# Kernel optimization log

Measured on AMD Instinct MI355X. Metric: run time of the kernel, lower is better.

The kernel has to match this reference:

```python
import jax, jax.numpy as jnp
import numpy as np

B, S, D, H = 4, 2048, 1024, 16
DH = D // H  # head dim = 64


def setup_inputs() -> dict:
    key = jax.random.key(0)
    ks = jax.random.split(key, 7)
    q = jax.random.normal(ks[0], (B, S, D), dtype=jnp.float32)
    k = jax.random.normal(ks[1], (B, S, D), dtype=jnp.float32)
    v = jax.random.normal(ks[2], (B, S, D), dtype=jnp.float32)
    mask = jax.random.uniform(ks[3], (1, S, S), dtype=jnp.float32)
    sc = 1.0 / np.sqrt(D)
    Wq = jax.random.normal(ks[4], (D, D), dtype=jnp.float32) * sc
    Wk = jax.random.normal(ks[5], (D, D), dtype=jnp.float32) * sc
    Wv = jax.random.normal(ks[6], (D, D), dtype=jnp.float32) * sc
    return {"q": q, "k": k, "v": v, "mask": mask, "Wq": Wq, "Wk": Wk, "Wv": Wv}


def reference(q, k, v, mask, Wq, Wk, Wv):
    # Linear projections (no bias), then split hidden into H heads.
    # tf.concat(tf.split(x, H, axis=2), axis=0) == reshape to (B,S,H,DH);
    # the final split/concat restores channel order [head0, head1, ...],
    # i.e. a plain (B,S,H,DH)->(B,S,D) reshape.
    qh = (q @ Wq).reshape(B, S, H, DH)
    kh = (k @ Wk).reshape(B, S, H, DH)
    vh = (v @ Wv).reshape(B, S, H, DH)
    score = jnp.einsum("bqhd,bkhd->bhqk", qh, kh) / jnp.sqrt(
        jnp.asarray(DH, dtype=q.dtype))
    # multiplicative mask applied BEFORE softmax (broadcast (1,Sq,Sk))
    score = score * mask[:, None, :, :][0:1].squeeze(0) if False else score * mask  # mask (1,Sq,Sk) broadcasts over (B,H,Sq,Sk)
    attn = jax.nn.softmax(score, axis=-1)
    out = jnp.einsum("bhqk,bkhd->bqhd", attn, vh).reshape(B, S, D)
    return out
```

## Files before the change

### kernel.cpp

```cpp
#include <hip/hip_runtime.h>

#define B_  4
#define S_  2048
#define D_  1024
#define H_  16
#define DH_ 64

typedef __attribute__((ext_vector_type(8))) short bf16x8;
typedef __attribute__((ext_vector_type(4))) float f32x4;
typedef __attribute__((ext_vector_type(4))) unsigned short u16x4;

__device__ __forceinline__ unsigned short f2bf(float f) {
  union { float f; unsigned int u; } x; x.f = f;
  unsigned int u = x.u;
  unsigned int r = (u + 0x7fffu + ((u >> 16) & 1u)) >> 16;
  return (unsigned short)r;
}

__device__ __forceinline__ int cvtpk(float lo, float hi) {
  unsigned r;
  asm("v_cvt_pk_bf16_f32 %0, %1, %2" : "=v"(r) : "v"(lo), "v"(hi));
  return (int)r;
}
__device__ __forceinline__ float bperm_f(int addr, float v) {
  union { float f; int i; } x; x.f = v;
  x.i = __builtin_amdgcn_ds_bpermute(addr, x.i);
  return x.f;
}

__global__ __launch_bounds__(256) void wtrans_kernel(const float* __restrict__ W0,
                                                     const float* __restrict__ W1,
                                                     const float* __restrict__ W2,
                                                     unsigned short* __restrict__ Wt) {
  __shared__ float t[32][33];
  const int z = blockIdx.z;
  const float* W = (z == 0) ? W0 : ((z == 1) ? W1 : W2);
  unsigned short* O = Wt + (size_t)z * (D_ * D_);
  const int n0 = blockIdx.x * 32, k0 = blockIdx.y * 32;
  const int tx = threadIdx.x, ty = threadIdx.y;
#pragma unroll
  for (int i = 0; i < 4; i++) t[ty + i * 8][tx] = W[(size_t)(k0 + ty + i * 8) * D_ + n0 + tx];
  __syncthreads();
#pragma unroll
  for (int i = 0; i < 4; i++)
    O[(size_t)(n0 + ty + i * 8) * D_ + k0 + tx] = f2bf(t[tx][ty + i * 8]);
}

__global__ __launch_bounds__(256) void proj_kernel(const float* __restrict__ X0,
                                                   const float* __restrict__ X1,
                                                   const float* __restrict__ X2,
                                                   const unsigned short* __restrict__ Wt,
                                                   unsigned short* __restrict__ Y0) {
  __shared__ unsigned short Alds[128 * 72];
  __shared__ unsigned short Blds[128 * 72];
  const int z = blockIdx.z;
  const float* X = (z == 0) ? X0 : ((z == 1) ? X1 : X2);
  const unsigned short* Wz = Wt + (size_t)z * (D_ * D_);
  unsigned short* Y = Y0 + (size_t)z * ((size_t)B_ * S_ * D_);

  const int tid = threadIdx.x;
  const int lane = tid & 63, w = tid >> 6;
  const int wr = w >> 1, wc = w & 1;
  const int l15 = lane & 15, lg = lane >> 4;
  const int r0 = blockIdx.y * 128, c0 = blockIdx.x * 128;

  f32x4 acc[4][4];
#pragma unroll
  for (int m = 0; m < 4; m++)
#pragma unroll
    for (int n = 0; n < 4; n++) acc[m][n] = (f32x4){0.f, 0.f, 0.f, 0.f};

  for (int kt = 0; kt < 16; ++kt) {
    __syncthreads();
    {
      const int rr = tid >> 4, cf = (tid & 15) * 4;
#pragma unroll
      for (int p = 0; p < 8; p++) {
        int row = rr + p * 16;
        float4 xv = *(const float4*)(X + (size_t)(r0 + row) * D_ + kt * 64 + cf);
        u16x4 bb = { f2bf(xv.x), f2bf(xv.y), f2bf(xv.z), f2bf(xv.w) };
        *(u16x4*)(&Alds[row * 72 + cf]) = bb;
      }
      const int rb = tid >> 3, cb = tid & 7;
#pragma unroll
      for (int p = 0; p < 4; p++) {
        int row = rb + p * 32;
        bf16x8 wv = *(const bf16x8*)(Wz + (size_t)(c0 + row) * D_ + kt * 64 + cb * 8);
        *(bf16x8*)(&Blds[row * 72 + cb * 8]) = wv;
      }
    }
    __syncthreads();

    bf16x8 af[4][2];
#pragma unroll
    for (int m = 0; m < 4; m++)
#pragma unroll
      for (int kc = 0; kc < 2; kc++)
        af[m][kc] = *(const bf16x8*)(&Alds[(wr * 64 + m * 16 + l15) * 72 + kc * 32 + lg * 8]);
#pragma unroll
    for (int n = 0; n < 4; n++) {
      bf16x8 bfr[2];
#pragma unroll
      for (int kc = 0; kc < 2; kc++)
        bfr[kc] = *(const bf16x8*)(&Blds[(wc * 64 + n * 16 + l15) * 72 + kc * 32 + lg * 8]);
#pragma unroll
      for (int m = 0; m < 4; m++)
#pragma unroll
        for (int kc = 0; kc < 2; kc++)
          acc[m][n] = __builtin_amdgcn_mfma_f32_16x16x32_bf16(af[m][kc], bfr[kc], acc[m][n], 0, 0, 0);
    }
  }

#pragma unroll
  for (int m = 0; m < 4; m++)
#pragma unroll
    for (int n = 0; n < 4; n++)
#pragma unroll
      for (int r = 0; r < 4; r++) {
        int row = r0 + wr * 64 + m * 16 + lg * 4 + r;
        int col = c0 + wc * 64 + n * 16 + l15;
        Y[(size_t)row * D_ + col] = f2bf(acc[m][n][r]);
      }
}

__global__ __launch_bounds__(256) void attn_kernel(
    const unsigned short* __restrict__ qh,
    const unsigned short* __restrict__ kh,
    const unsigned short* __restrict__ vh,
    const float* __restrict__ mask,
    float* __restrict__ out) {
  __shared__ __align__(16) unsigned short K_lds[2][64 * 72];
  __shared__ __align__(16) unsigned short V_lds[2][64 * 72];

  const int tid = threadIdx.x;
  const int lane = tid & 63, w = tid >> 6;
  const int l15 = lane & 15, lg = lane >> 4;
  const int q0 = blockIdx.x * 64;
  const int h = blockIdx.y, b = blockIdx.z;
  const size_t head = (size_t)b * S_ * D_ + h * DH_;

  bf16x8 bq[2];
  {
    const unsigned short* qp = qh + head + (size_t)(q0 + w * 16 + l15) * D_;
#pragma unroll
    for (int kc = 0; kc < 2; kc++) bq[kc] = *(const bf16x8*)(qp + kc * 32 + lg * 8);
  }

  const int rr = tid >> 3, cc = tid & 7;
  const unsigned short* kbase = kh + head + (size_t)rr * D_ + cc * 8;
  const unsigned short* vbase = vh + head + (size_t)rr * D_ + cc * 8;

  const int aL0 = (((lg & 1) * 32 + l15) << 2);
  const int aL1 = aL0 + 64;
  const int selhi = lg >> 1;
  int badr[4];
#pragma unroll
  for (int r = 0; r < 4; r++) badr[r] = (lg * 16 + lg * 4 + r) << 2;

  f32x4 o_acc[4];
#pragma unroll
  for (int dn = 0; dn < 4; dn++) o_acc[dn] = (f32x4){0.f, 0.f, 0.f, 0.f};
  float m_r = -INFINITY, l_r = 0.f;

  bf16x8 kreg[2], vreg[2];
#pragma unroll
  for (int p = 0; p < 2; p++) {
    kreg[p] = *(const bf16x8*)(kbase + (size_t)p * 32 * D_);
    vreg[p] = *(const bf16x8*)(vbase + (size_t)p * 32 * D_);
  }
#pragma unroll
  for (int p = 0; p < 2; p++) {
    int row = rr + p * 32;
    *(bf16x8*)(&K_lds[0][row * 72 + cc * 8]) = kreg[p];
#pragma unroll
    for (int j = 0; j < 8; j++) {
      int d = cc * 8 + j;
      int byt = (d * 72 + row) * 2;
      byt ^= ((d >> 3) & 7) << 4;
      *(unsigned short*)((char*)&V_lds[0][0] + byt) = (unsigned short)vreg[p][j];
    }
  }

  const float cs = 0.125f * 1.44269504f;

  for (int kt = 0; kt < 32; kt++) {
    const int cur = kt & 1;

    bf16x8 kreg2[2], vreg2[2];
    if (kt + 1 < 32) {
      const size_t tb = (size_t)(kt + 1) * 64 * D_;
#pragma unroll
      for (int p = 0; p < 2; p++) {
        kreg2[p] = *(const bf16x8*)(kbase + tb + (size_t)p * 32 * D_);
        vreg2[p] = *(const bf16x8*)(vbase + tb + (size_t)p * 32 * D_);
      }
    }

    __syncthreads();

    f32x4 sacc[4];
#pragma unroll
    for (int kn = 0; kn < 4; kn++) sacc[kn] = (f32x4){0.f, 0.f, 0.f, 0.f};
#pragma unroll
    for (int kc = 0; kc < 2; kc++)
#pragma unroll
      for (int kn = 0; kn < 4; kn++) {
        bf16x8 ak = *(const bf16x8*)(&K_lds[cur][(kn * 16 + l15) * 72 + kc * 32 + lg * 8]);
        sacc[kn] = __builtin_amdgcn_mfma_f32_16x16x32_bf16(ak, bq[kc], sacc[kn], 0, 0, 0);
      }

    float sl[16];
    const float* mrow = mask + (size_t)(q0 + w * 16 + l15) * S_ + kt * 64 + lg * 4;
#pragma unroll
    for (int kn = 0; kn < 4; kn++) {
      float4 mk = *(const float4*)(mrow + kn * 16);
      sl[kn * 4 + 0] = sacc[kn][0] * (cs * mk.x);
      sl[kn * 4 + 1] = sacc[kn][1] * (cs * mk.y);
      sl[kn * 4 + 2] = sacc[kn][2] * (cs * mk.z);
      sl[kn * 4 + 3] = sacc[kn][3] * (cs * mk.w);
    }

    float tm = sl[0];
#pragma unroll
    for (int i = 1; i < 16; i++) tm = fmaxf(tm, sl[i]);
    tm = fmaxf(tm, __shfl_xor(tm, 16));
    tm = fmaxf(tm, __shfl_xor(tm, 32));

    float mn;
    if (__any(tm > m_r + 8.0f)) {
      mn = fmaxf(m_r, tm);
      float alpha = exp2f(m_r - mn);
      m_r = mn;
      l_r *= alpha;
#pragma unroll
      for (int r = 0; r < 4; r++) {
        float ao = bperm_f(badr[r], alpha);
#pragma unroll
        for (int dn = 0; dn < 4; dn++) o_acc[dn][r] *= ao;
      }
    } else {
      mn = m_r;
    }

    float rs = 0.f;
#pragma unroll
    for (int i = 0; i < 16; i++) {
      float p = exp2f(sl[i] - mn);
      sl[i] = p;
      rs += p;
    }
    rs += __shfl_xor(rs, 16);
    rs += __shfl_xor(rs, 32);
    l_r += rs;

    int pw[8];
#pragma unroll
    for (int kn = 0; kn < 4; kn++) {
      pw[kn * 2 + 0] = cvtpk(sl[kn * 4 + 0], sl[kn * 4 + 1]);
      pw[kn * 2 + 1] = cvtpk(sl[kn * 4 + 2], sl[kn * 4 + 3]);
    }
    bf16x8 af[2];
#pragma unroll
    for (int kc = 0; kc < 2; kc++) {
      int pA0 = pw[(kc * 2 + 0) * 2 + 0], pA1 = pw[(kc * 2 + 0) * 2 + 1];
      int pB0 = pw[(kc * 2 + 1) * 2 + 0], pB1 = pw[(kc * 2 + 1) * 2 + 1];
      int a0 = __builtin_amdgcn_ds_bpermute(aL0, pA0);
      int b0 = __builtin_amdgcn_ds_bpermute(aL0, pB0);
      int a1 = __builtin_amdgcn_ds_bpermute(aL0, pA1);
      int b1 = __builtin_amdgcn_ds_bpermute(aL0, pB1);
      int a2 = __builtin_amdgcn_ds_bpermute(aL1, pA0);
      int b2 = __builtin_amdgcn_ds_bpermute(aL1, pB0);
      int a3 = __builtin_amdgcn_ds_bpermute(aL1, pA1);
      int b3 = __builtin_amdgcn_ds_bpermute(aL1, pB1);
      union { int u[4]; bf16x8 v; } cv;
      cv.u[0] = selhi ? b0 : a0;
      cv.u[1] = selhi ? b1 : a1;
      cv.u[2] = selhi ? b2 : a2;
      cv.u[3] = selhi ? b3 : a3;
      af[kc] = cv.v;
    }

#pragma unroll
    for (int kc = 0; kc < 2; kc++)
#pragma unroll
      for (int dn = 0; dn < 4; dn++) {
        int dc = dn * 16 + l15;
        int byt = (dc * 72 + kc * 32 + lg * 8) * 2;
        byt ^= ((dc >> 3) & 7) << 4;
        bf16x8 bv = *(const bf16x8*)((const char*)&V_lds[cur][0] + byt);
        o_acc[dn] = __builtin_amdgcn_mfma_f32_16x16x32_bf16(af[kc], bv, o_acc[dn], 0, 0, 0);
      }

    if (kt + 1 < 32) {
#pragma unroll
      for (int p = 0; p < 2; p++) {
        int row = rr + p * 32;
        *(bf16x8*)(&K_lds[cur ^ 1][row * 72 + cc * 8]) = kreg2[p];
#pragma unroll
        for (int j = 0; j < 8; j++) {
          int d = cc * 8 + j;
          int byt = (d * 72 + row) * 2;
          byt ^= ((d >> 3) & 7) << 4;
          *(unsigned short*)((char*)&V_lds[cur ^ 1][0] + byt) = (unsigned short)vreg2[p][j];
        }
      }
    }
  }

  float inv[4];
#pragma unroll
  for (int r = 0; r < 4; r++) inv[r] = 1.0f / bperm_f(badr[r], l_r);
  float* op = out + (size_t)(b * S_ + q0 + w * 16) * D_ + h * DH_;
#pragma unroll
  for (int dn = 0; dn < 4; dn++)
#pragma unroll
    for (int r = 0; r < 4; r++)
      op[(size_t)(lg * 4 + r) * D_ + dn * 16 + l15] = o_acc[dn][r] * inv[r];
}

extern "C" void kernel_launch(void* const* d_in, const int* in_sizes, int n_in,
                              void* d_out, int out_size, void* d_ws, size_t ws_size,
                              hipStream_t stream) {
  const float* q = (const float*)d_in[0];
  const float* k = (const float*)d_in[1];
  const float* v = (const float*)d_in[2];
  const float* mask = (const float*)d_in[3];
  const float* Wq = (const float*)d_in[4];
  const float* Wk = (const float*)d_in[5];
  const float* Wv = (const float*)d_in[6];

  char* ws = (char*)d_ws;
  const size_t SZ_PROJ = (size_t)B_ * S_ * D_ * 2;
  unsigned short* qh = (unsigned short*)(ws);
  unsigned short* kh = (unsigned short*)(ws + SZ_PROJ);
  unsigned short* vh = (unsigned short*)(ws + 2 * SZ_PROJ);
  unsigned short* Wt = (unsigned short*)(ws + 3 * SZ_PROJ);

  wtrans_kernel<<<dim3(D_ / 32, D_ / 32, 3), dim3(32, 8), 0, stream>>>(Wq, Wk, Wv, Wt);
  proj_kernel<<<dim3(D_ / 128, (B_ * S_) / 128, 3), 256, 0, stream>>>(q, k, v, Wt, qh);
  attn_kernel<<<dim3(S_ / 64, H_, B_), 256, 0, stream>>>(qh, kh, vh, mask, (float*)d_out);
}
```

Baseline: 344.3 us.

## Process two 16-row query groups per wave to double K/V tile reuse

Each attention block now covers 128 query rows instead of 64, with every wave holding two independent 16-row query groups that keep their own online-softmax state. Each K/V tile loaded into LDS and each fragment read from LDS now feeds twice as many MFMAs, halving K/V global traffic and LDS staging per query. The costs are more registers per thread (two sets of accumulators and softmax state), which may lower occupancy, and half as many blocks (1024) to spread over the compute units.

```diff
diff --git a/kernel.cpp b/kernel.cpp
--- a/kernel.cpp
+++ b/kernel.cpp
@@ -135,15 +135,16 @@
   const int tid = threadIdx.x;
   const int lane = tid & 63, w = tid >> 6;
   const int l15 = lane & 15, lg = lane >> 4;
-  const int q0 = blockIdx.x * 64;
+  const int q0 = blockIdx.x * 128;
   const int h = blockIdx.y, b = blockIdx.z;
   const size_t head = (size_t)b * S_ * D_ + h * DH_;
 
-  bf16x8 bq[2];
-  {
-    const unsigned short* qp = qh + head + (size_t)(q0 + w * 16 + l15) * D_;
-#pragma unroll
-    for (int kc = 0; kc < 2; kc++) bq[kc] = *(const bf16x8*)(qp + kc * 32 + lg * 8);
+  bf16x8 bq[2][2];
+#pragma unroll
+  for (int g = 0; g < 2; g++) {
+    const unsigned short* qp = qh + head + (size_t)(q0 + w * 32 + g * 16 + l15) * D_;
+#pragma unroll
+    for (int kc = 0; kc < 2; kc++) bq[g][kc] = *(const bf16x8*)(qp + kc * 32 + lg * 8);
   }
 
   const int rr = tid >> 3, cc = tid & 7;
@@ -157,10 +158,12 @@
 #pragma unroll
   for (int r = 0; r < 4; r++) badr[r] = (lg * 16 + lg * 4 + r) << 2;
 
-  f32x4 o_acc[4];
-#pragma unroll
-  for (int dn = 0; dn < 4; dn++) o_acc[dn] = (f32x4){0.f, 0.f, 0.f, 0.f};
-  float m_r = -INFINITY, l_r = 0.f;
+  f32x4 o_acc[2][4];
+#pragma unroll
+  for (int g = 0; g < 2; g++)
+#pragma unroll
+    for (int dn = 0; dn < 4; dn++) o_acc[g][dn] = (f32x4){0.f, 0.f, 0.f, 0.f};
+  float m_r[2] = {-INFINITY, -INFINITY}, l_r[2] = {0.f, 0.f};
 
   bf16x8 kreg[2], vreg[2];
 #pragma unroll
@@ -198,86 +201,92 @@
 
     __syncthreads();
 
-    f32x4 sacc[4];
-#pragma unroll
-    for (int kn = 0; kn < 4; kn++) sacc[kn] = (f32x4){0.f, 0.f, 0.f, 0.f};
+    f32x4 sacc[2][4];
+#pragma unroll
+    for (int g = 0; g < 2; g++)
+#pragma unroll
+      for (int kn = 0; kn < 4; kn++) sacc[g][kn] = (f32x4){0.f, 0.f, 0.f, 0.f};
 #pragma unroll
     for (int kc = 0; kc < 2; kc++)
 #pragma unroll
       for (int kn = 0; kn < 4; kn++) {
         bf16x8 ak = *(const bf16x8*)(&K_lds[cur][(kn * 16 + l15) * 72 + kc * 32 + lg * 8]);
-        sacc[kn] = __builtin_amdgcn_mfma_f32_16x16x32_bf16(ak, bq[kc], sacc[kn], 0, 0, 0);
-      }
-
-    float sl[16];
-    const float* mrow = mask + (size_t)(q0 + w * 16 + l15) * S_ + kt * 64 + lg * 4;
-#pragma unroll
-    for (int kn = 0; kn < 4; kn++) {
-      float4 mk = *(const float4*)(mrow + kn * 16);
-      sl[kn * 4 + 0] = sacc[kn][0] * (cs * mk.x);
-      sl[kn * 4 + 1] = sacc[kn][1] * (cs * mk.y);
-      sl[kn * 4 + 2] = sacc[kn][2] * (cs * mk.z);
-      sl[kn * 4 + 3] = sacc[kn][3] * (cs * mk.w);
-    }
-
-    float tm = sl[0];
-#pragma unroll
-    for (int i = 1; i < 16; i++) tm = fmaxf(tm, sl[i]);
-    tm = fmaxf(tm, __shfl_xor(tm, 16));
-    tm = fmaxf(tm, __shfl_xor(tm, 32));
-
-    float mn;
-    if (__any(tm > m_r + 8.0f)) {
-      mn = fmaxf(m_r, tm);
-      float alpha = exp2f(m_r - mn);
-      m_r = mn;
-      l_r *= alpha;
-#pragma unroll
-      for (int r = 0; r < 4; r++) {
-        float ao = bperm_f(badr[r], alpha);
-#pragma unroll
-        for (int dn = 0; dn < 4; dn++) o_acc[dn][r] *= ao;
-      }
-    } else {
-      mn = m_r;
-    }
-
-    float rs = 0.f;
-#pragma unroll
-    for (int i = 0; i < 16; i++) {
-      float p = exp2f(sl[i] - mn);
-      sl[i] = p;
-      rs += p;
-    }
-    rs += __shfl_xor(rs, 16);
-    rs += __shfl_xor(rs, 32);
-    l_r += rs;
-
-    int pw[8];
-#pragma unroll
-    for (int kn = 0; kn < 4; kn++) {
-      pw[kn * 2 + 0] = cvtpk(sl[kn * 4 + 0], sl[kn * 4 + 1]);
-      pw[kn * 2 + 1] = cvtpk(sl[kn * 4 + 2], sl[kn * 4 + 3]);
-    }
-    bf16x8 af[2];
-#pragma unroll
-    for (int kc = 0; kc < 2; kc++) {
-      int pA0 = pw[(kc * 2 + 0) * 2 + 0], pA1 = pw[(kc * 2 + 0) * 2 + 1];
-      int pB0 = pw[(kc * 2 + 1) * 2 + 0], pB1 = pw[(kc * 2 + 1) * 2 + 1];
-      int a0 = __builtin_amdgcn_ds_bpermute(aL0, pA0);
-      int b0 = __builtin_amdgcn_ds_bpermute(aL0, pB0);
-      int a1 = __builtin_amdgcn_ds_bpermute(aL0, pA1);
-      int b1 = __builtin_amdgcn_ds_bpermute(aL0, pB1);
-      int a2 = __builtin_amdgcn_ds_bpermute(aL1, pA0);
-      int b2 = __builtin_amdgcn_ds_bpermute(aL1, pB0);
-      int a3 = __builtin_amdgcn_ds_bpermute(aL1, pA1);
-      int b3 = __builtin_amdgcn_ds_bpermute(aL1, pB1);
-      union { int u[4]; bf16x8 v; } cv;
-      cv.u[0] = selhi ? b0 : a0;
-      cv.u[1] = selhi ? b1 : a1;
-      cv.u[2] = selhi ? b2 : a2;
-      cv.u[3] = selhi ? b3 : a3;
-      af[kc] = cv.v;
+        sacc[0][kn] = __builtin_amdgcn_mfma_f32_16x16x32_bf16(ak, bq[0][kc], sacc[0][kn], 0, 0, 0);
+        sacc[1][kn] = __builtin_amdgcn_mfma_f32_16x16x32_bf16(ak, bq[1][kc], sacc[1][kn], 0, 0, 0);
+      }
+
+    bf16x8 af[2][2];
+#pragma unroll
+    for (int g = 0; g < 2; g++) {
+      float sl[16];
+      const float* mrow = mask + (size_t)(q0 + w * 32 + g * 16 + l15) * S_ + kt * 64 + lg * 4;
+#pragma unroll
+      for (int kn = 0; kn < 4; kn++) {
+        float4 mk = *(const float4*)(mrow + kn * 16);
+        sl[kn * 4 + 0] = sacc[g][kn][0] * (cs * mk.x);
+        sl[kn * 4 + 1] = sacc[g][kn][1] * (cs * mk.y);
+        sl[kn * 4 + 2] = sacc[g][kn][2] * (cs * mk.z);
+        sl[kn * 4 + 3] = sacc[g][kn][3] * (cs * mk.w);
+      }
+
+      float tm = sl[0];
+#pragma unroll
+      for (int i = 1; i < 16; i++) tm = fmaxf(tm, sl[i]);
+      tm = fmaxf(tm, __shfl_xor(tm, 16));
+      tm = fmaxf(tm, __shfl_xor(tm, 32));
+
+      float mn;
+      if (__any(tm > m_r[g] + 8.0f)) {
+        mn = fmaxf(m_r[g], tm);
+        float alpha = exp2f(m_r[g] - mn);
+        m_r[g] = mn;
+        l_r[g] *= alpha;
+#pragma unroll
+        for (int r = 0; r < 4; r++) {
+          float ao = bperm_f(badr[r], alpha);
+#pragma unroll
+          for (int dn = 0; dn < 4; dn++) o_acc[g][dn][r] *= ao;
+        }
+      } else {
+        mn = m_r[g];
+      }
+
+      float rs = 0.f;
+#pragma unroll
+      for (int i = 0; i < 16; i++) {
+        float p = exp2f(sl[i] - mn);
+        sl[i] = p;
+        rs += p;
+      }
+      rs += __shfl_xor(rs, 16);
+      rs += __shfl_xor(rs, 32);
+      l_r[g] += rs;
+
+      int pw[8];
+#pragma unroll
+      for (int kn = 0; kn < 4; kn++) {
+        pw[kn * 2 + 0] = cvtpk(sl[kn * 4 + 0], sl[kn * 4 + 1]);
+        pw[kn * 2 + 1] = cvtpk(sl[kn * 4 + 2], sl[kn * 4 + 3]);
+      }
+#pragma unroll
+      for (int kc = 0; kc < 2; kc++) {
+        int pA0 = pw[(kc * 2 + 0) * 2 + 0], pA1 = pw[(kc * 2 + 0) * 2 + 1];
+        int pB0 = pw[(kc * 2 + 1) * 2 + 0], pB1 = pw[(kc * 2 + 1) * 2 + 1];
+        int a0 = __builtin_amdgcn_ds_bpermute(aL0, pA0);
+        int b0 = __builtin_amdgcn_ds_bpermute(aL0, pB0);
+        int a1 = __builtin_amdgcn_ds_bpermute(aL0, pA1);
+        int b1 = __builtin_amdgcn_ds_bpermute(aL0, pB1);
+        int a2 = __builtin_amdgcn_ds_bpermute(aL1, pA0);
+        int b2 = __builtin_amdgcn_ds_bpermute(aL1, pB0);
+        int a3 = __builtin_amdgcn_ds_bpermute(aL1, pA1);
+        int b3 = __builtin_amdgcn_ds_bpermute(aL1, pB1);
+        union { int u[4]; bf16x8 v; } cv;
+        cv.u[0] = selhi ? b0 : a0;
+        cv.u[1] = selhi ? b1 : a1;
+        cv.u[2] = selhi ? b2 : a2;
+        cv.u[3] = selhi ? b3 : a3;
+        af[g][kc] = cv.v;
+      }
     }
 
 #pragma unroll
@@ -288,7 +297,8 @@
         int byt = (dc * 72 + kc * 32 + lg * 8) * 2;
         byt ^= ((dc >> 3) & 7) << 4;
         bf16x8 bv = *(const bf16x8*)((const char*)&V_lds[cur][0] + byt);
-        o_acc[dn] = __builtin_amdgcn_mfma_f32_16x16x32_bf16(af[kc], bv, o_acc[dn], 0, 0, 0);
+        o_acc[0][dn] = __builtin_amdgcn_mfma_f32_16x16x32_bf16(af[0][kc], bv, o_acc[0][dn], 0, 0, 0);
+        o_acc[1][dn] = __builtin_amdgcn_mfma_f32_16x16x32_bf16(af[1][kc], bv, o_acc[1][dn], 0, 0, 0);
       }
 
     if (kt + 1 < 32) {
@@ -307,15 +317,18 @@
     }
   }
 
-  float inv[4];
-#pragma unroll
-  for (int r = 0; r < 4; r++) inv[r] = 1.0f / bperm_f(badr[r], l_r);
-  float* op = out + (size_t)(b * S_ + q0 + w * 16) * D_ + h * DH_;
-#pragma unroll
-  for (int dn = 0; dn < 4; dn++)
-#pragma unroll
-    for (int r = 0; r < 4; r++)
-      op[(size_t)(lg * 4 + r) * D_ + dn * 16 + l15] = o_acc[dn][r] * inv[r];
+#pragma unroll
+  for (int g = 0; g < 2; g++) {
+    float inv[4];
+#pragma unroll
+    for (int r = 0; r < 4; r++) inv[r] = 1.0f / bperm_f(badr[r], l_r[g]);
+    float* op = out + (size_t)(b * S_ + q0 + w * 32 + g * 16) * D_ + h * DH_;
+#pragma unroll
+    for (int dn = 0; dn < 4; dn++)
+#pragma unroll
+      for (int r = 0; r < 4; r++)
+        op[(size_t)(lg * 4 + r) * D_ + dn * 16 + l15] = o_acc[g][dn][r] * inv[r];
+  }
 }
 
 extern "C" void kernel_launch(void* const* d_in, const int* in_sizes, int n_in,
@@ -338,5 +351,5 @@
 
   wtrans_kernel<<<dim3(D_ / 32, D_ / 32, 3), dim3(32, 8), 0, stream>>>(Wq, Wk, Wv, Wt);
   proj_kernel<<<dim3(D_ / 128, (B_ * S_) / 128, 3), 256, 0, stream>>>(q, k, v, Wt, qh);
-  attn_kernel<<<dim3(S_ / 64, H_, B_), 256, 0, stream>>>(qh, kh, vh, mask, (float*)d_out);
-}
+  attn_kernel<<<dim3(S_ / 128, H_, B_), 256, 0, stream>>>(qh, kh, vh, mask, (float*)d_out);
+}
```

New measurement: 323.4 us. -6.1%, faster.

## Switch attention to 32x32x16 MFMA with 128-query tiles and fold scale into Q

Applied to the files above, without the earlier changes.

Rewrites the attention kernel to use 32x32x16 bf16 MFMA, with each wave owning 32 query rows. Each block now covers 128 queries, so every loaded K/V tile is reused by twice as many queries. The 1/sqrt(dh)*log2e scale is folded into the Q projection epilogue. Per-row softmax stats now sit in one lane, which removes the bpermute-based alpha/l broadcasts, and outputs are written as float4 stores. The trade-offs are larger accumulators (higher register pressure), half as many blocks, and slightly different rounding from scaling before the bf16 conversion.

```diff
diff --git a/kernel.cpp b/kernel.cpp
--- a/kernel.cpp
+++ b/kernel.cpp
@@ -8,6 +8,7 @@
 
 typedef __attribute__((ext_vector_type(8))) short bf16x8;
 typedef __attribute__((ext_vector_type(4))) float f32x4;
+typedef __attribute__((ext_vector_type(16))) float f32x16;
 typedef __attribute__((ext_vector_type(4))) unsigned short u16x4;
 
 __device__ __forceinline__ unsigned short f2bf(float f) {
@@ -21,11 +22,6 @@
   unsigned r;
   asm("v_cvt_pk_bf16_f32 %0, %1, %2" : "=v"(r) : "v"(lo), "v"(hi));
   return (int)r;
-}
-__device__ __forceinline__ float bperm_f(int addr, float v) {
-  union { float f; int i; } x; x.f = v;
-  x.i = __builtin_amdgcn_ds_bpermute(addr, x.i);
-  return x.f;
 }
 
 __global__ __launch_bounds__(256) void wtrans_kernel(const float* __restrict__ W0,
@@ -57,6 +53,7 @@
   const float* X = (z == 0) ? X0 : ((z == 1) ? X1 : X2);
   const unsigned short* Wz = Wt + (size_t)z * (D_ * D_);
   unsigned short* Y = Y0 + (size_t)z * ((size_t)B_ * S_ * D_);
+  const float osc = (z == 0) ? 0.18033688f : 1.0f;
 
   const int tid = threadIdx.x;
   const int lane = tid & 63, w = tid >> 6;
@@ -119,7 +116,7 @@
       for (int r = 0; r < 4; r++) {
         int row = r0 + wr * 64 + m * 16 + lg * 4 + r;
         int col = c0 + wc * 64 + n * 16 + l15;
-        Y[(size_t)row * D_ + col] = f2bf(acc[m][n][r]);
+        Y[(size_t)row * D_ + col] = f2bf(acc[m][n][r] * osc);
       }
 }
 
@@ -134,32 +131,28 @@
 
   const int tid = threadIdx.x;
   const int lane = tid & 63, w = tid >> 6;
-  const int l15 = lane & 15, lg = lane >> 4;
-  const int q0 = blockIdx.x * 64;
+  const int l31 = lane & 31, hf = lane >> 5;
+  const int q0 = blockIdx.x * 128;
   const int h = blockIdx.y, b = blockIdx.z;
   const size_t head = (size_t)b * S_ * D_ + h * DH_;
-
-  bf16x8 bq[2];
+  const int qrow = q0 + w * 32 + l31;
+
+  bf16x8 bq[4];
   {
-    const unsigned short* qp = qh + head + (size_t)(q0 + w * 16 + l15) * D_;
-#pragma unroll
-    for (int kc = 0; kc < 2; kc++) bq[kc] = *(const bf16x8*)(qp + kc * 32 + lg * 8);
+    const unsigned short* qp = qh + head + (size_t)qrow * D_;
+#pragma unroll
+    for (int ds = 0; ds < 4; ds++) bq[ds] = *(const bf16x8*)(qp + ds * 16 + hf * 8);
   }
 
   const int rr = tid >> 3, cc = tid & 7;
   const unsigned short* kbase = kh + head + (size_t)rr * D_ + cc * 8;
   const unsigned short* vbase = vh + head + (size_t)rr * D_ + cc * 8;
 
-  const int aL0 = (((lg & 1) * 32 + l15) << 2);
-  const int aL1 = aL0 + 64;
-  const int selhi = lg >> 1;
-  int badr[4];
-#pragma unroll
-  for (int r = 0; r < 4; r++) badr[r] = (lg * 16 + lg * 4 + r) << 2;
-
-  f32x4 o_acc[4];
-#pragma unroll
-  for (int dn = 0; dn < 4; dn++) o_acc[dn] = (f32x4){0.f, 0.f, 0.f, 0.f};
+  f32x16 o_acc[2];
+#pragma unroll
+  for (int dt = 0; dt < 2; dt++)
+#pragma unroll
+    for (int r = 0; r < 16; r++) o_acc[dt][r] = 0.f;
   float m_r = -INFINITY, l_r = 0.f;
 
   bf16x8 kreg[2], vreg[2];
@@ -181,8 +174,6 @@
     }
   }
 
-  const float cs = 0.125f * 1.44269504f;
-
   for (int kt = 0; kt < 32; kt++) {
     const int cur = kt & 1;
 
@@ -198,32 +189,36 @@
 
     __syncthreads();
 
-    f32x4 sacc[4];
-#pragma unroll
-    for (int kn = 0; kn < 4; kn++) sacc[kn] = (f32x4){0.f, 0.f, 0.f, 0.f};
-#pragma unroll
-    for (int kc = 0; kc < 2; kc++)
-#pragma unroll
-      for (int kn = 0; kn < 4; kn++) {
-        bf16x8 ak = *(const bf16x8*)(&K_lds[cur][(kn * 16 + l15) * 72 + kc * 32 + lg * 8]);
-        sacc[kn] = __builtin_amdgcn_mfma_f32_16x16x32_bf16(ak, bq[kc], sacc[kn], 0, 0, 0);
-      }
-
-    float sl[16];
-    const float* mrow = mask + (size_t)(q0 + w * 16 + l15) * S_ + kt * 64 + lg * 4;
-#pragma unroll
-    for (int kn = 0; kn < 4; kn++) {
-      float4 mk = *(const float4*)(mrow + kn * 16);
-      sl[kn * 4 + 0] = sacc[kn][0] * (cs * mk.x);
-      sl[kn * 4 + 1] = sacc[kn][1] * (cs * mk.y);
-      sl[kn * 4 + 2] = sacc[kn][2] * (cs * mk.z);
-      sl[kn * 4 + 3] = sacc[kn][3] * (cs * mk.w);
-    }
-
-    float tm = sl[0];
-#pragma unroll
-    for (int i = 1; i < 16; i++) tm = fmaxf(tm, sl[i]);
-    tm = fmaxf(tm, __shfl_xor(tm, 16));
+    f32x16 sacc[2];
+#pragma unroll
+    for (int ct = 0; ct < 2; ct++)
+#pragma unroll
+      for (int r = 0; r < 16; r++) sacc[ct][r] = 0.f;
+#pragma unroll
+    for (int ds = 0; ds < 4; ds++)
+#pragma unroll
+      for (int ct = 0; ct < 2; ct++) {
+        bf16x8 ak = *(const bf16x8*)(&K_lds[cur][(ct * 32 + l31) * 72 + ds * 16 + hf * 8]);
+        sacc[ct] = __builtin_amdgcn_mfma_f32_32x32x16_bf16(ak, bq[ds], sacc[ct], 0, 0, 0);
+      }
+
+    const float* mrow = mask + (size_t)qrow * S_ + kt * 64 + hf * 4;
+#pragma unroll
+    for (int ct = 0; ct < 2; ct++)
+#pragma unroll
+      for (int rq = 0; rq < 4; rq++) {
+        float4 mk = *(const float4*)(mrow + ct * 32 + rq * 8);
+        sacc[ct][rq * 4 + 0] *= mk.x;
+        sacc[ct][rq * 4 + 1] *= mk.y;
+        sacc[ct][rq * 4 + 2] *= mk.z;
+        sacc[ct][rq * 4 + 3] *= mk.w;
+      }
+
+    float tm = sacc[0][0];
+#pragma unroll
+    for (int r = 1; r < 16; r++) tm = fmaxf(tm, sacc[0][r]);
+#pragma unroll
+    for (int r = 0; r < 16; r++) tm = fmaxf(tm, sacc[1][r]);
     tm = fmaxf(tm, __shfl_xor(tm, 32));
 
     float mn;
@@ -233,63 +228,55 @@
       m_r = mn;
       l_r *= alpha;
 #pragma unroll
-      for (int r = 0; r < 4; r++) {
-        float ao = bperm_f(badr[r], alpha);
-#pragma unroll
-        for (int dn = 0; dn < 4; dn++) o_acc[dn][r] *= ao;
-      }
+      for (int dt = 0; dt < 2; dt++)
+#pragma unroll
+        for (int r = 0; r < 16; r++) o_acc[dt][r] *= alpha;
     } else {
       mn = m_r;
     }
 
     float rs = 0.f;
 #pragma unroll
-    for (int i = 0; i < 16; i++) {
-      float p = exp2f(sl[i] - mn);
-      sl[i] = p;
-      rs += p;
-    }
-    rs += __shfl_xor(rs, 16);
+    for (int ct = 0; ct < 2; ct++)
+#pragma unroll
+      for (int r = 0; r < 16; r++) {
+        float p = exp2f(sacc[ct][r] - mn);
+        sacc[ct][r] = p;
+        rs += p;
+      }
     rs += __shfl_xor(rs, 32);
     l_r += rs;
 
-    int pw[8];
-#pragma unroll
-    for (int kn = 0; kn < 4; kn++) {
-      pw[kn * 2 + 0] = cvtpk(sl[kn * 4 + 0], sl[kn * 4 + 1]);
-      pw[kn * 2 + 1] = cvtpk(sl[kn * 4 + 2], sl[kn * 4 + 3]);
-    }
-    bf16x8 af[2];
-#pragma unroll
-    for (int kc = 0; kc < 2; kc++) {
-      int pA0 = pw[(kc * 2 + 0) * 2 + 0], pA1 = pw[(kc * 2 + 0) * 2 + 1];
-      int pB0 = pw[(kc * 2 + 1) * 2 + 0], pB1 = pw[(kc * 2 + 1) * 2 + 1];
-      int a0 = __builtin_amdgcn_ds_bpermute(aL0, pA0);
-      int b0 = __builtin_amdgcn_ds_bpermute(aL0, pB0);
-      int a1 = __builtin_amdgcn_ds_bpermute(aL0, pA1);
-      int b1 = __builtin_amdgcn_ds_bpermute(aL0, pB1);
-      int a2 = __builtin_amdgcn_ds_bpermute(aL1, pA0);
-      int b2 = __builtin_amdgcn_ds_bpermute(aL1, pB0);
-      int a3 = __builtin_amdgcn_ds_bpermute(aL1, pA1);
-      int b3 = __builtin_amdgcn_ds_bpermute(aL1, pB1);
+    bf16x8 bfp[4];
+#pragma unroll
+    for (int s = 0; s < 4; s++) {
+      const int ct = s >> 1, rb = (s & 1) * 8;
+      int L1 = cvtpk(sacc[ct][rb + 0], sacc[ct][rb + 1]);
+      int L2 = cvtpk(sacc[ct][rb + 2], sacc[ct][rb + 3]);
+      int H1 = cvtpk(sacc[ct][rb + 4], sacc[ct][rb + 5]);
+      int H2 = cvtpk(sacc[ct][rb + 6], sacc[ct][rb + 7]);
+      int xL1 = __shfl_xor(L1, 32), xL2 = __shfl_xor(L2, 32);
+      int xH1 = __shfl_xor(H1, 32), xH2 = __shfl_xor(H2, 32);
       union { int u[4]; bf16x8 v; } cv;
-      cv.u[0] = selhi ? b0 : a0;
-      cv.u[1] = selhi ? b1 : a1;
-      cv.u[2] = selhi ? b2 : a2;
-      cv.u[3] = selhi ? b3 : a3;
-      af[kc] = cv.v;
-    }
-
-#pragma unroll
-    for (int kc = 0; kc < 2; kc++)
-#pragma unroll
-      for (int dn = 0; dn < 4; dn++) {
-        int dc = dn * 16 + l15;
-        int byt = (dc * 72 + kc * 32 + lg * 8) * 2;
-        byt ^= ((dc >> 3) & 7) << 4;
-        bf16x8 bv = *(const bf16x8*)((const char*)&V_lds[cur][0] + byt);
-        o_acc[dn] = __builtin_amdgcn_mfma_f32_16x16x32_bf16(af[kc], bv, o_acc[dn], 0, 0, 0);
-      }
+      cv.u[0] = hf ? xH1 : L1;
+      cv.u[1] = hf ? xH2 : L2;
+      cv.u[2] = hf ? H1 : xL1;
+      cv.u[3] = hf ? H2 : xL2;
+      bfp[s] = cv.v;
+    }
+
+#pragma unroll
+    for (int dt = 0; dt < 2; dt++) {
+      const int d0 = dt * 32 + l31;
+      const int bbase = d0 * 144;
+      const int swz = ((d0 >> 3) & 7) << 4;
+#pragma unroll
+      for (int s = 0; s < 4; s++) {
+        int byt = (bbase + (s * 16 + hf * 8) * 2) ^ swz;
+        bf16x8 av = *(const bf16x8*)((const char*)&V_lds[cur][0] + byt);
+        o_acc[dt] = __builtin_amdgcn_mfma_f32_32x32x16_bf16(av, bfp[s], o_acc[dt], 0, 0, 0);
+      }
+    }
 
     if (kt + 1 < 32) {
 #pragma unroll
@@ -307,15 +294,16 @@
     }
   }
 
-  float inv[4];
-#pragma unroll
-  for (int r = 0; r < 4; r++) inv[r] = 1.0f / bperm_f(badr[r], l_r);
-  float* op = out + (size_t)(b * S_ + q0 + w * 16) * D_ + h * DH_;
-#pragma unroll
-  for (int dn = 0; dn < 4; dn++)
-#pragma unroll
-    for (int r = 0; r < 4; r++)
-      op[(size_t)(lg * 4 + r) * D_ + dn * 16 + l15] = o_acc[dn][r] * inv[r];
+  const float invl = 1.0f / l_r;
+  float* op = out + (size_t)(b * S_ + qrow) * D_ + h * DH_;
+#pragma unroll
+  for (int dt = 0; dt < 2; dt++)
+#pragma unroll
+    for (int rq = 0; rq < 4; rq++) {
+      float4 ov = { o_acc[dt][rq * 4 + 0] * invl, o_acc[dt][rq * 4 + 1] * invl,
+                    o_acc[dt][rq * 4 + 2] * invl, o_acc[dt][rq * 4 + 3] * invl };
+      *(float4*)(op + dt * 32 + rq * 8 + hf * 4) = ov;
+    }
 }
 
 extern "C" void kernel_launch(void* const* d_in, const int* in_sizes, int n_in,
@@ -338,5 +326,5 @@
 
   wtrans_kernel<<<dim3(D_ / 32, D_ / 32, 3), dim3(32, 8), 0, stream>>>(Wq, Wk, Wv, Wt);
   proj_kernel<<<dim3(D_ / 128, (B_ * S_) / 128, 3), 256, 0, stream>>>(q, k, v, Wt, qh);
-  attn_kernel<<<dim3(S_ / 64, H_, B_), 256, 0, stream>>>(qh, kh, vh, mask, (float*)d_out);
-}
+  attn_kernel<<<dim3(S_ / 128, H_, B_), 256, 0, stream>>>(qh, kh, vh, mask, (float*)d_out);
+}
```

New measurement: 343.1 us. Within noise of the previous version (-0.3%).
